# Performance work log

Measured on AMD Instinct MI355X. Metric: run time of the kernel, lower is better.

## Reference

```python
import jax, jax.numpy as jnp
import numpy as np

N_NODES = 100000

def setup_inputs() -> dict:
    key = jax.random.key(0)
    k = jax.random.split(key, 6)
    N, E, D = N_NODES, 1600000, 128
    x = jax.random.normal(k[0], (N, D), dtype=jnp.float32)
    edge_src = jax.random.randint(k[1], (E,), 0, N, dtype=jnp.int32)
    edge_dst = jax.random.randint(k[2], (E,), 0, N, dtype=jnp.int32)
    edge_weight = jax.random.uniform(k[3], (E,), dtype=jnp.float32)
    W1 = jax.random.normal(k[4], (D, D), dtype=jnp.float32) * (1.0 / np.sqrt(D))
    W2 = jax.random.normal(k[5], (D, D), dtype=jnp.float32) * (1.0 / np.sqrt(D))
    return {"x": x, "edge_src": edge_src, "edge_dst": edge_dst,
            "edge_weight": edge_weight, "W1": W1, "W2": W2}

def _graph_conv(x, W, src, dst, ew, n_nodes):
    # GraphConv: h = A @ (x @ W); A given as weighted edge list.
    h = x @ W                               # [N, D_out]
    msg = h[src] * ew[:, None]              # [E, D_out] gather + scale
    return jax.ops.segment_sum(msg, dst, num_segments=n_nodes)  # [N, D_out]

def reference(x, edge_src, edge_dst, edge_weight, W1, W2):
    n = x.shape[0]
    # layer 1: tanh(GraphConv) ; Dropout(0) is identity
    x = jnp.tanh(_graph_conv(x, W1, edge_src, edge_dst, edge_weight, n))
    # layer 2
    x = jnp.tanh(_graph_conv(x, W2, edge_src, edge_dst, edge_weight, n))
    return x
```

## Files before the change

### kernel.cpp

```cpp
#include <hip/hip_runtime.h>
#include <hip/hip_bf16.h>

#define N_NODES 100000
#define N_EDGES 1600000
#define D 128
#define BSZ 128
#define NBUCK 782
#define EPW 4096
#define NWG1 ((N_EDGES + EPW - 1) / EPW)
#define CAP 4096
#define OTS 272

typedef unsigned int  uint4n  __attribute__((ext_vector_type(4)));
typedef float         float4n __attribute__((ext_vector_type(4)));
typedef _Float16      half8n  __attribute__((ext_vector_type(8)));
typedef _Float16      half4n  __attribute__((ext_vector_type(4)));

#define SWZ(row, kb) (((row) << 8) + ((kb) ^ (((row) & 15) << 4)))

__device__ __forceinline__ float fast_tanh(float x) {
    float t = __builtin_amdgcn_exp2f(x * 2.885390081777927f);
    return 1.0f - 2.0f * __builtin_amdgcn_rcpf(t + 1.0f);
}

__global__ __launch_bounds__(256) void k_wprep_hist(const float* __restrict__ W1,
                                                    const float* __restrict__ W2,
                                                    char* __restrict__ Wt,
                                                    const int* __restrict__ dst,
                                                    int* __restrict__ bcnt) {
    if (blockIdx.x < 32) {
        const float* W = (blockIdx.x < 16) ? W1 : W2;
        char* dstp = Wt + ((blockIdx.x < 16) ? 0 : 32768);
        int t = (blockIdx.x & 15) * 256 + threadIdx.x;
        int idx = t * 4;
        int k = idx >> 7, c = idx & 127;
        float4 wv = *(const float4*)&W[idx];
        *(_Float16*)(dstp + SWZ(c + 0, k * 2)) = (_Float16)wv.x;
        *(_Float16*)(dstp + SWZ(c + 1, k * 2)) = (_Float16)wv.y;
        *(_Float16*)(dstp + SWZ(c + 2, k * 2)) = (_Float16)wv.z;
        *(_Float16*)(dstp + SWZ(c + 3, k * 2)) = (_Float16)wv.w;
        return;
    }
    __shared__ int h[NBUCK];
    for (int i = threadIdx.x; i < NBUCK; i += 256) h[i] = 0;
    __syncthreads();
    int hb   = blockIdx.x - 32;
    int base = hb * EPW;
    int end  = min(base + EPW, N_EDGES);
    int i = base + threadIdx.x;
    for (; i + 768 < end; i += 1024) {
        int d0 = dst[i], d1 = dst[i + 256], d2 = dst[i + 512], d3 = dst[i + 768];
        atomicAdd(&h[d0 >> 7], 1);
        atomicAdd(&h[d1 >> 7], 1);
        atomicAdd(&h[d2 >> 7], 1);
        atomicAdd(&h[d3 >> 7], 1);
    }
    for (; i < end; i += 256)
        atomicAdd(&h[dst[i] >> 7], 1);
    __syncthreads();
    for (int j = threadIdx.x; j < NBUCK; j += 256)
        if (h[j]) atomicAdd(&bcnt[j], h[j]);
}

__global__ void k_scanN(const int* __restrict__ bcnt, int* __restrict__ boff,
                        int* __restrict__ gcur) {
    __shared__ int tmp[256];
    int tid = threadIdx.x;
    int carry = 0;
    for (int c = 0; c < (NBUCK + 255) / 256; c++) {
        int i = c * 256 + tid;
        int v = (i < NBUCK) ? bcnt[i] : 0;
        tmp[tid] = v;
        __syncthreads();
        int run = v;
        for (int off = 1; off < 256; off <<= 1) {
            int t = (tid >= off) ? tmp[tid - off] : 0;
            __syncthreads();
            run += t;
            tmp[tid] = run;
            __syncthreads();
        }
        int excl = carry + run - v;
        if (i < NBUCK) { boff[i] = excl; gcur[i] = excl; }
        int tot = tmp[255];
        __syncthreads();
        carry += tot;
    }
    if (tid == 0) boff[NBUCK] = N_EDGES;
}

__global__ __launch_bounds__(256) void k_scat_gemm(const int* __restrict__ src,
                                                   const int* __restrict__ dst,
                                                   const float* __restrict__ ew,
                                                   int* __restrict__ gcur,
                                                   int2* __restrict__ ebuf,
                                                   const float* __restrict__ Xf,
                                                   const char* __restrict__ Wt,
                                                   _Float16* __restrict__ H, int n) {
    __shared__ char smem[17408];
    int tid = threadIdx.x;

    if (blockIdx.x < NWG1) {
        int* h  = (int*)smem;
        int* rb = h + NBUCK;
        for (int i = tid; i < NBUCK; i += 256) h[i] = 0;
        __syncthreads();
        int base = blockIdx.x * EPW;
        int end  = min(base + EPW, N_EDGES);
        {
            int i = base + tid;
            for (; i + 768 < end; i += 1024) {
                int d0 = dst[i], d1 = dst[i + 256], d2 = dst[i + 512], d3 = dst[i + 768];
                atomicAdd(&h[d0 >> 7], 1);
                atomicAdd(&h[d1 >> 7], 1);
                atomicAdd(&h[d2 >> 7], 1);
                atomicAdd(&h[d3 >> 7], 1);
            }
            for (; i < end; i += 256)
                atomicAdd(&h[dst[i] >> 7], 1);
        }
        __syncthreads();
        for (int i = tid; i < NBUCK; i += 256) {
            int c = h[i];
            if (c) rb[i] = atomicAdd(&gcur[i], c);
        }
        __syncthreads();
        {
            int i = base + tid;
            for (; i + 768 < end; i += 1024) {
                int d0 = dst[i], d1 = dst[i + 256], d2 = dst[i + 512], d3 = dst[i + 768];
                int s0 = src[i], s1 = src[i + 256], s2 = src[i + 512], s3 = src[i + 768];
                float w0 = ew[i], w1 = ew[i + 256], w2 = ew[i + 512], w3 = ew[i + 768];
                int p0 = atomicAdd(&rb[d0 >> 7], 1);
                int p1 = atomicAdd(&rb[d1 >> 7], 1);
                int p2 = atomicAdd(&rb[d2 >> 7], 1);
                int p3 = atomicAdd(&rb[d3 >> 7], 1);
                ebuf[p0] = make_int2((s0 << 8) | (d0 & 127), __float_as_int(w0));
                ebuf[p1] = make_int2((s1 << 8) | (d1 & 127), __float_as_int(w1));
                ebuf[p2] = make_int2((s2 << 8) | (d2 & 127), __float_as_int(w2));
                ebuf[p3] = make_int2((s3 << 8) | (d3 & 127), __float_as_int(w3));
            }
            for (; i < end; i += 256) {
                int d = dst[i];
                int p = atomicAdd(&rb[d >> 7], 1);
                ebuf[p] = make_int2((src[i] << 8) | (d & 127), __float_as_int(ew[i]));
            }
        }
        return;
    }

    char* sA = smem;
    int lane = tid & 63, w = tid >> 6;
    int rows0 = (blockIdx.x - NWG1) * 64;

    int rb2 = (w >> 1) * 32;
    int cb = (w & 1) * 64;
    int lr = lane & 15;
    int kg = (lane >> 4) * 16;

    #pragma unroll
    for (int rep = 0; rep < 8; rep++) {
        int ef = rep * 1024 + tid * 4;
        int r = ef >> 7, c = ef & 127;
        int rg = rows0 + r;
        float4 xv = make_float4(0.f, 0.f, 0.f, 0.f);
        if (rg < n) xv = *(const float4*)(Xf + (size_t)rg * 128 + c);
        half4n hv;
        hv[0] = (_Float16)xv.x; hv[1] = (_Float16)xv.y;
        hv[2] = (_Float16)xv.z; hv[3] = (_Float16)xv.w;
        *(half4n*)(sA + SWZ(r, c * 2)) = hv;
    }
    __syncthreads();

    float4n acc[2][4] = {};
    #pragma unroll
    for (int ks = 0; ks < 4; ks++) {
        half8n bwk[4];
        #pragma unroll
        for (int ct = 0; ct < 4; ct++)
            bwk[ct] = *(const half8n*)(Wt + SWZ(cb + ct * 16 + lr, ks * 64 + kg));
        half8n af[2];
        #pragma unroll
        for (int rt = 0; rt < 2; rt++)
            af[rt] = *(const half8n*)(sA + SWZ(rb2 + rt * 16 + lr, ks * 64 + kg));
        #pragma unroll
        for (int rt = 0; rt < 2; rt++)
            #pragma unroll
            for (int ct = 0; ct < 4; ct++)
                acc[rt][ct] = __builtin_amdgcn_mfma_f32_16x16x32_f16(af[rt], bwk[ct], acc[rt][ct], 0, 0, 0);
    }

    __syncthreads();
    char* OT = smem;
    int rloc = rb2 + (lane >> 4) * 4;
    #pragma unroll
    for (int rt = 0; rt < 2; rt++) {
        #pragma unroll
        for (int ct = 0; ct < 4; ct++) {
            int col = cb + ct * 16 + lr;
            #pragma unroll
            for (int r = 0; r < 4; r++)
                *(_Float16*)(OT + (rloc + rt * 16 + r) * OTS + col * 2) = (_Float16)acc[rt][ct][r];
        }
    }
    __syncthreads();
    #pragma unroll
    for (int rep = 0; rep < 4; rep++) {
        int ef = rep * 2048 + tid * 8;
        int r = ef >> 7, c = ef & 127;
        int rg = rows0 + r;
        if (rg < n) {
            half8n v = *(const half8n*)(OT + r * OTS + c * 2);
            *(half8n*)&H[(size_t)rg * 128 + c] = v;
        }
    }
}

__global__ __launch_bounds__(512) void k_sortb(int2* __restrict__ ebuf,
                                               const int* __restrict__ boff,
                                               int* __restrict__ rowptr) {
    __shared__ int2 se[CAP];
    __shared__ int cnt[BSZ];
    __shared__ int cur[BSZ];
    int tid = threadIdx.x;
    int b   = blockIdx.x;
    int e0 = boff[b], e1 = boff[b + 1];
    int m  = e1 - e0;
    if (tid < BSZ) cnt[tid] = 0;
    __syncthreads();
    int2 ovf;
    bool hasOvf = false;
    for (int i = tid; i < m; i += 512) {
        int2 v = ebuf[e0 + i];
        if (i < CAP) se[i] = v;
        else { ovf = v; hasOvf = true; }
        atomicAdd(&cnt[v.x & (BSZ - 1)], 1);
    }
    __syncthreads();
    if (tid < 64) {
        int a  = cnt[tid * 2], bq = cnt[tid * 2 + 1];
        int s  = a + bq;
        int incl = s;
        #pragma unroll
        for (int off = 1; off < 64; off <<= 1) {
            int t = __shfl_up(incl, off, 64);
            if (tid >= off) incl += t;
        }
        int ex = incl - s;
        cur[tid * 2]     = ex;
        cur[tid * 2 + 1] = ex + a;
        int node = b * BSZ + tid * 2;
        if (node     <= N_NODES) rowptr[node]     = e0 + ex;
        if (node + 1 <= N_NODES) rowptr[node + 1] = e0 + ex + a;
    }
    __syncthreads();
    for (int i = tid; i < m && i < CAP; i += 512) {
        int2 v = se[i];
        int p = atomicAdd(&cur[v.x & (BSZ - 1)], 1);
        ebuf[e0 + p] = v;
    }
    if (hasOvf) {
        int p = atomicAdd(&cur[ovf.x & (BSZ - 1)], 1);
        ebuf[e0 + p] = ovf;
    }
}

__global__ __launch_bounds__(256) void k_gemm2(const _Float16* __restrict__ Xh,
                                               const char* __restrict__ Wt,
                                               _Float16* __restrict__ H, int n) {
    __shared__ char smem[17408];
    char* sA = smem;
    int tid  = threadIdx.x;
    int lane = tid & 63, w = tid >> 6;
    int rows0 = blockIdx.x * 64;

    int rb = (w >> 1) * 32;
    int cb = (w & 1) * 64;
    int lr = lane & 15;
    int kg = (lane >> 4) * 16;

    #pragma unroll
    for (int rep = 0; rep < 4; rep++) {
        int ef = rep * 2048 + tid * 8;
        int r = ef >> 7, c = ef & 127;
        int rg = rows0 + r;
        half8n v = half8n(0);
        if (rg < n) v = *(const half8n*)(Xh + (size_t)rg * 128 + c);
        *(half8n*)(sA + SWZ(r, c * 2)) = v;
    }
    __syncthreads();

    float4n acc[2][4] = {};
    #pragma unroll
    for (int ks = 0; ks < 4; ks++) {
        half8n bwk[4];
        #pragma unroll
        for (int ct = 0; ct < 4; ct++)
            bwk[ct] = *(const half8n*)(Wt + SWZ(cb + ct * 16 + lr, ks * 64 + kg));
        half8n af[2];
        #pragma unroll
        for (int rt = 0; rt < 2; rt++)
            af[rt] = *(const half8n*)(sA + SWZ(rb + rt * 16 + lr, ks * 64 + kg));
        #pragma unroll
        for (int rt = 0; rt < 2; rt++)
            #pragma unroll
            for (int ct = 0; ct < 4; ct++)
                acc[rt][ct] = __builtin_amdgcn_mfma_f32_16x16x32_f16(af[rt], bwk[ct], acc[rt][ct], 0, 0, 0);
    }

    __syncthreads();
    char* OT = smem;
    int rloc = rb + (lane >> 4) * 4;
    #pragma unroll
    for (int rt = 0; rt < 2; rt++) {
        #pragma unroll
        for (int ct = 0; ct < 4; ct++) {
            int col = cb + ct * 16 + lr;
            #pragma unroll
            for (int r = 0; r < 4; r++)
                *(_Float16*)(OT + (rloc + rt * 16 + r) * OTS + col * 2) = (_Float16)acc[rt][ct][r];
        }
    }
    __syncthreads();
    #pragma unroll
    for (int rep = 0; rep < 4; rep++) {
        int ef = rep * 2048 + tid * 8;
        int r = ef >> 7, c = ef & 127;
        int rg = rows0 + r;
        if (rg < n) {
            half8n v = *(const half8n*)(OT + r * OTS + c * 2);
            *(half8n*)&H[(size_t)rg * 128 + c] = v;
        }
    }
}

template<bool OUTF16>
__global__ __launch_bounds__(256) void k_agg(const _Float16* __restrict__ H,
                                             const int* __restrict__ rowptr,
                                             const int2* __restrict__ ebuf,
                                             void* __restrict__ outv, int n) {
    int wv   = (blockIdx.x * 256 + threadIdx.x) >> 6;
    int lane = threadIdx.x & 63;
    int g = lane >> 4;
    int c = lane & 15;
    int node = wv * 4 + g;
    if (node >= n) return;
    const char* Hc = (const char*)H + (c << 4);
    int e0 = rowptr[node], e1 = rowptr[node + 1];
    float acc[8] = {};
    int e = e0;
    for (; e + 4 <= e1; e += 4) {
        int2 d0 = ebuf[e];
        int2 d1 = ebuf[e + 1];
        int2 d2 = ebuf[e + 2];
        int2 d3 = ebuf[e + 3];
        half8n v0 = *(const half8n*)(Hc + (size_t)((unsigned)d0.x & 0xFFFFFF00u));
        half8n v1 = *(const half8n*)(Hc + (size_t)((unsigned)d1.x & 0xFFFFFF00u));
        half8n v2 = *(const half8n*)(Hc + (size_t)((unsigned)d2.x & 0xFFFFFF00u));
        half8n v3 = *(const half8n*)(Hc + (size_t)((unsigned)d3.x & 0xFFFFFF00u));
        float w0 = __int_as_float(d0.y);
        float w1 = __int_as_float(d1.y);
        float w2 = __int_as_float(d2.y);
        float w3 = __int_as_float(d3.y);
        #pragma unroll
        for (int j = 0; j < 8; j++) acc[j] = __builtin_fmaf((float)v0[j], w0, acc[j]);
        #pragma unroll
        for (int j = 0; j < 8; j++) acc[j] = __builtin_fmaf((float)v1[j], w1, acc[j]);
        #pragma unroll
        for (int j = 0; j < 8; j++) acc[j] = __builtin_fmaf((float)v2[j], w2, acc[j]);
        #pragma unroll
        for (int j = 0; j < 8; j++) acc[j] = __builtin_fmaf((float)v3[j], w3, acc[j]);
    }
    for (; e < e1; ++e) {
        int2 ed = ebuf[e];
        half8n v = *(const half8n*)(Hc + (size_t)((unsigned)ed.x & 0xFFFFFF00u));
        float w = __int_as_float(ed.y);
        #pragma unroll
        for (int j = 0; j < 8; j++) acc[j] = __builtin_fmaf((float)v[j], w, acc[j]);
    }
    if (OUTF16) {
        half8n hv;
        #pragma unroll
        for (int j = 0; j < 8; j++) hv[j] = (_Float16)fast_tanh(acc[j]);
        *(uint4n*)((_Float16*)outv + (size_t)node * 128 + c * 8) = *(uint4n*)&hv;
    } else {
        float* op = (float*)outv + (size_t)node * 128 + c * 8;
        float4n o0, o1;
        o0.x = fast_tanh(acc[0]); o0.y = fast_tanh(acc[1]);
        o0.z = fast_tanh(acc[2]); o0.w = fast_tanh(acc[3]);
        o1.x = fast_tanh(acc[4]); o1.y = fast_tanh(acc[5]);
        o1.z = fast_tanh(acc[6]); o1.w = fast_tanh(acc[7]);
        __builtin_nontemporal_store(o0, (float4n*)op);
        __builtin_nontemporal_store(o1, (float4n*)(op + 4));
    }
}


extern "C" void kernel_launch(void* const* d_in, const int* in_sizes, int n_in,
                              void* d_out, int out_size, void* d_ws, size_t ws_size,
                              hipStream_t stream) {
    const float* x    = (const float*)d_in[0];
    const int*   esrc = (const int*)d_in[1];
    const int*   edst = (const int*)d_in[2];
    const float* ew   = (const float*)d_in[3];
    const float* W1   = (const float*)d_in[4];
    const float* W2   = (const float*)d_in[5];
    float* out = (float*)d_out;

    _Float16* hbuf = (_Float16*)d_ws;
    _Float16* act1 = hbuf + (size_t)N_NODES * D;
    int2* ebuf     = (int2*)(act1 + (size_t)N_NODES * D);
    int*  bcnt     = (int*)(ebuf + N_EDGES);
    int*  boff     = bcnt + NBUCK;
    int*  gcur     = boff + (NBUCK + 1);
    int*  rowptr   = gcur + NBUCK;
    char* Wt       = (char*)(rowptr + N_NODES + 8);
    (void)ws_size; (void)in_sizes; (void)n_in; (void)out_size;

    int gemm_blocks = (N_NODES + 63) / 64;
    int agg_blocks  = (N_NODES + 15) / 16;

    hipMemsetAsync(bcnt, 0, NBUCK * sizeof(int), stream);
    k_wprep_hist<<<32 + NWG1, 256, 0, stream>>>(W1, W2, Wt, edst, bcnt);
    k_scanN<<<1, 256, 0, stream>>>(bcnt, boff, gcur);
    k_scat_gemm<<<NWG1 + gemm_blocks, 256, 0, stream>>>(esrc, edst, ew, gcur, ebuf,
                                                        x, Wt, hbuf, N_NODES);
    k_sortb<<<NBUCK, 512, 0, stream>>>(ebuf, boff, rowptr);

    k_agg<true><<<agg_blocks, 256, 0, stream>>>(hbuf, rowptr, ebuf, act1, N_NODES);
    k_gemm2<<<gemm_blocks, 256, 0, stream>>>(act1, Wt + 32768, hbuf, N_NODES);
    k_agg<false><<<agg_blocks, 256, 0, stream>>>(hbuf, rowptr, ebuf, out, N_NODES);
}
```

Measured before the change: 219.3 us.

## Replace global histogram+atomic scatter with per-block local bucketing and staged merge

Removes the separate global histogram pass, memset and global atomic cursor. Instead each scatter block locally scans its bucket histogram and writes records to a private staging region, recording per-block counts and offsets. New column-sum and scan kernels compute the bucket offsets, and the sort kernel gathers each bucket's records from all blocks using a binary search over per-block prefix counts. This drops one full pass over dst and the global atomics, at the cost of more kernels, a 256-step in-block scan per scatter block, and a binary search per record in the sort.

```diff
diff --git a/kernel.cpp b/kernel.cpp
--- a/kernel.cpp
+++ b/kernel.cpp
@@ -23,77 +23,27 @@
     return 1.0f - 2.0f * __builtin_amdgcn_rcpf(t + 1.0f);
 }
 
-__global__ __launch_bounds__(256) void k_wprep_hist(const float* __restrict__ W1,
-                                                    const float* __restrict__ W2,
-                                                    char* __restrict__ Wt,
-                                                    const int* __restrict__ dst,
-                                                    int* __restrict__ bcnt) {
-    if (blockIdx.x < 32) {
-        const float* W = (blockIdx.x < 16) ? W1 : W2;
-        char* dstp = Wt + ((blockIdx.x < 16) ? 0 : 32768);
-        int t = (blockIdx.x & 15) * 256 + threadIdx.x;
-        int idx = t * 4;
-        int k = idx >> 7, c = idx & 127;
-        float4 wv = *(const float4*)&W[idx];
-        *(_Float16*)(dstp + SWZ(c + 0, k * 2)) = (_Float16)wv.x;
-        *(_Float16*)(dstp + SWZ(c + 1, k * 2)) = (_Float16)wv.y;
-        *(_Float16*)(dstp + SWZ(c + 2, k * 2)) = (_Float16)wv.z;
-        *(_Float16*)(dstp + SWZ(c + 3, k * 2)) = (_Float16)wv.w;
-        return;
-    }
-    __shared__ int h[NBUCK];
-    for (int i = threadIdx.x; i < NBUCK; i += 256) h[i] = 0;
-    __syncthreads();
-    int hb   = blockIdx.x - 32;
-    int base = hb * EPW;
-    int end  = min(base + EPW, N_EDGES);
-    int i = base + threadIdx.x;
-    for (; i + 768 < end; i += 1024) {
-        int d0 = dst[i], d1 = dst[i + 256], d2 = dst[i + 512], d3 = dst[i + 768];
-        atomicAdd(&h[d0 >> 7], 1);
-        atomicAdd(&h[d1 >> 7], 1);
-        atomicAdd(&h[d2 >> 7], 1);
-        atomicAdd(&h[d3 >> 7], 1);
-    }
-    for (; i < end; i += 256)
-        atomicAdd(&h[dst[i] >> 7], 1);
-    __syncthreads();
-    for (int j = threadIdx.x; j < NBUCK; j += 256)
-        if (h[j]) atomicAdd(&bcnt[j], h[j]);
-}
-
-__global__ void k_scanN(const int* __restrict__ bcnt, int* __restrict__ boff,
-                        int* __restrict__ gcur) {
-    __shared__ int tmp[256];
-    int tid = threadIdx.x;
-    int carry = 0;
-    for (int c = 0; c < (NBUCK + 255) / 256; c++) {
-        int i = c * 256 + tid;
-        int v = (i < NBUCK) ? bcnt[i] : 0;
-        tmp[tid] = v;
-        __syncthreads();
-        int run = v;
-        for (int off = 1; off < 256; off <<= 1) {
-            int t = (tid >= off) ? tmp[tid - off] : 0;
-            __syncthreads();
-            run += t;
-            tmp[tid] = run;
-            __syncthreads();
-        }
-        int excl = carry + run - v;
-        if (i < NBUCK) { boff[i] = excl; gcur[i] = excl; }
-        int tot = tmp[255];
-        __syncthreads();
-        carry += tot;
-    }
-    if (tid == 0) boff[NBUCK] = N_EDGES;
+__global__ __launch_bounds__(256) void k_wprep(const float* __restrict__ W1,
+                                               const float* __restrict__ W2,
+                                               char* __restrict__ Wt) {
+    const float* W = (blockIdx.x < 16) ? W1 : W2;
+    char* dstp = Wt + ((blockIdx.x < 16) ? 0 : 32768);
+    int t = (blockIdx.x & 15) * 256 + threadIdx.x;
+    int idx = t * 4;
+    int k = idx >> 7, c = idx & 127;
+    float4 wv = *(const float4*)&W[idx];
+    *(_Float16*)(dstp + SWZ(c + 0, k * 2)) = (_Float16)wv.x;
+    *(_Float16*)(dstp + SWZ(c + 1, k * 2)) = (_Float16)wv.y;
+    *(_Float16*)(dstp + SWZ(c + 2, k * 2)) = (_Float16)wv.z;
+    *(_Float16*)(dstp + SWZ(c + 3, k * 2)) = (_Float16)wv.w;
 }
 
 __global__ __launch_bounds__(256) void k_scat_gemm(const int* __restrict__ src,
                                                    const int* __restrict__ dst,
                                                    const float* __restrict__ ew,
-                                                   int* __restrict__ gcur,
-                                                   int2* __restrict__ ebuf,
+                                                   int2* __restrict__ staging,
+                                                   int* __restrict__ cntM,
+                                                   int* __restrict__ loffM,
                                                    const float* __restrict__ Xf,
                                                    const char* __restrict__ Wt,
                                                    _Float16* __restrict__ H, int n) {
@@ -101,11 +51,13 @@
     int tid = threadIdx.x;
 
     if (blockIdx.x < NWG1) {
-        int* h  = (int*)smem;
-        int* rb = h + NBUCK;
+        int* h   = (int*)smem;
+        int* cur = h + NBUCK;
+        int* tmp = cur + NBUCK;
+        int blk  = blockIdx.x;
         for (int i = tid; i < NBUCK; i += 256) h[i] = 0;
         __syncthreads();
-        int base = blockIdx.x * EPW;
+        int base = blk * EPW;
         int end  = min(base + EPW, N_EDGES);
         {
             int i = base + tid;
@@ -120,30 +72,51 @@
                 atomicAdd(&h[dst[i] >> 7], 1);
         }
         __syncthreads();
-        for (int i = tid; i < NBUCK; i += 256) {
-            int c = h[i];
-            if (c) rb[i] = atomicAdd(&gcur[i], c);
+        int carry = 0;
+        for (int c = 0; c < 4; c++) {
+            int i = c * 256 + tid;
+            int v = (i < NBUCK) ? h[i] : 0;
+            tmp[tid] = v;
+            __syncthreads();
+            int run = v;
+            for (int off = 1; off < 256; off <<= 1) {
+                int t = (tid >= off) ? tmp[tid - off] : 0;
+                __syncthreads();
+                run += t;
+                tmp[tid] = run;
+                __syncthreads();
+            }
+            int excl = carry + run - v;
+            if (i < NBUCK) {
+                cur[i] = excl;
+                cntM[blk * NBUCK + i]  = v;
+                loffM[blk * NBUCK + i] = excl;
+            }
+            int tot = tmp[255];
+            __syncthreads();
+            carry += tot;
         }
         __syncthreads();
         {
+            int2* sg = staging + (size_t)blk * EPW;
             int i = base + tid;
             for (; i + 768 < end; i += 1024) {
                 int d0 = dst[i], d1 = dst[i + 256], d2 = dst[i + 512], d3 = dst[i + 768];
                 int s0 = src[i], s1 = src[i + 256], s2 = src[i + 512], s3 = src[i + 768];
                 float w0 = ew[i], w1 = ew[i + 256], w2 = ew[i + 512], w3 = ew[i + 768];
-                int p0 = atomicAdd(&rb[d0 >> 7], 1);
-                int p1 = atomicAdd(&rb[d1 >> 7], 1);
-                int p2 = atomicAdd(&rb[d2 >> 7], 1);
-                int p3 = atomicAdd(&rb[d3 >> 7], 1);
-                ebuf[p0] = make_int2((s0 << 8) | (d0 & 127), __float_as_int(w0));
-                ebuf[p1] = make_int2((s1 << 8) | (d1 & 127), __float_as_int(w1));
-                ebuf[p2] = make_int2((s2 << 8) | (d2 & 127), __float_as_int(w2));
-                ebuf[p3] = make_int2((s3 << 8) | (d3 & 127), __float_as_int(w3));
+                int p0 = atomicAdd(&cur[d0 >> 7], 1);
+                int p1 = atomicAdd(&cur[d1 >> 7], 1);
+                int p2 = atomicAdd(&cur[d2 >> 7], 1);
+                int p3 = atomicAdd(&cur[d3 >> 7], 1);
+                sg[p0] = make_int2((s0 << 8) | (d0 & 127), __float_as_int(w0));
+                sg[p1] = make_int2((s1 << 8) | (d1 & 127), __float_as_int(w1));
+                sg[p2] = make_int2((s2 << 8) | (d2 & 127), __float_as_int(w2));
+                sg[p3] = make_int2((s3 << 8) | (d3 & 127), __float_as_int(w3));
             }
             for (; i < end; i += 256) {
                 int d = dst[i];
-                int p = atomicAdd(&rb[d >> 7], 1);
-                ebuf[p] = make_int2((src[i] << 8) | (d & 127), __float_as_int(ew[i]));
+                int p = atomicAdd(&cur[d >> 7], 1);
+                sg[p] = make_int2((src[i] << 8) | (d & 127), __float_as_int(ew[i]));
             }
         }
         return;
@@ -216,29 +189,91 @@
     }
 }
 
-__global__ __launch_bounds__(512) void k_sortb(int2* __restrict__ ebuf,
+__global__ __launch_bounds__(256) void k_sumcol(const int* __restrict__ cntM,
+                                                int* __restrict__ bcnt) {
+    int b = blockIdx.x * 256 + threadIdx.x;
+    if (b >= NBUCK) return;
+    int s = 0;
+    int blk = 0;
+    for (; blk + 4 <= NWG1; blk += 4) {
+        int a0 = cntM[(size_t)(blk + 0) * NBUCK + b];
+        int a1 = cntM[(size_t)(blk + 1) * NBUCK + b];
+        int a2 = cntM[(size_t)(blk + 2) * NBUCK + b];
+        int a3 = cntM[(size_t)(blk + 3) * NBUCK + b];
+        s += a0 + a1 + a2 + a3;
+    }
+    for (; blk < NWG1; blk++) s += cntM[(size_t)blk * NBUCK + b];
+    bcnt[b] = s;
+}
+
+__global__ void k_scanN(const int* __restrict__ bcnt, int* __restrict__ boff) {
+    __shared__ int tmp[256];
+    int tid = threadIdx.x;
+    int carry = 0;
+    for (int c = 0; c < (NBUCK + 255) / 256; c++) {
+        int i = c * 256 + tid;
+        int v = (i < NBUCK) ? bcnt[i] : 0;
+        tmp[tid] = v;
+        __syncthreads();
+        int run = v;
+        for (int off = 1; off < 256; off <<= 1) {
+            int t = (tid >= off) ? tmp[tid - off] : 0;
+            __syncthreads();
+            run += t;
+            tmp[tid] = run;
+            __syncthreads();
+        }
+        int excl = carry + run - v;
+        if (i < NBUCK) boff[i] = excl;
+        int tot = tmp[255];
+        __syncthreads();
+        carry += tot;
+    }
+    if (tid == 0) boff[NBUCK] = N_EDGES;
+}
+
+__global__ __launch_bounds__(512) void k_sortb(const int2* __restrict__ staging,
+                                               const int* __restrict__ cntM,
+                                               const int* __restrict__ loffM,
                                                const int* __restrict__ boff,
+                                               int2* __restrict__ ebuf,
                                                int* __restrict__ rowptr) {
     __shared__ int2 se[CAP];
-    __shared__ int cnt[BSZ];
-    __shared__ int cur[BSZ];
+    __shared__ int rcs[512];
+    __shared__ int rco[512];
+    __shared__ int lfs[NWG1];
+    __shared__ int cnt2[BSZ];
+    __shared__ int cur2[BSZ];
     int tid = threadIdx.x;
     int b   = blockIdx.x;
     int e0 = boff[b], e1 = boff[b + 1];
     int m  = e1 - e0;
-    if (tid < BSZ) cnt[tid] = 0;
-    __syncthreads();
-    int2 ovf;
-    bool hasOvf = false;
+    {
+        int v = (tid < NWG1) ? cntM[(size_t)tid * NBUCK + b] : 0;
+        rcs[tid] = v;
+        rco[tid] = v;
+        if (tid < NWG1) lfs[tid] = loffM[(size_t)tid * NBUCK + b];
+        if (tid < BSZ) cnt2[tid] = 0;
+    }
+    __syncthreads();
+    for (int off = 1; off < 512; off <<= 1) {
+        int t = (tid >= off) ? rcs[tid - off] : 0;
+        __syncthreads();
+        rcs[tid] += t;
+        __syncthreads();
+    }
     for (int i = tid; i < m; i += 512) {
-        int2 v = ebuf[e0 + i];
-        if (i < CAP) se[i] = v;
-        else { ovf = v; hasOvf = true; }
-        atomicAdd(&cnt[v.x & (BSZ - 1)], 1);
+        int lo = 0, hi = NWG1 - 1;
+        while (lo < hi) { int mid = (lo + hi) >> 1; if (rcs[mid] > i) hi = mid; else lo = mid + 1; }
+        int blk = lo;
+        int within = i - (rcs[blk] - rco[blk]);
+        int2 rec = staging[(size_t)blk * EPW + lfs[blk] + within];
+        if (i < CAP) se[i] = rec;
+        atomicAdd(&cnt2[rec.x & (BSZ - 1)], 1);
     }
     __syncthreads();
     if (tid < 64) {
-        int a  = cnt[tid * 2], bq = cnt[tid * 2 + 1];
+        int a  = cnt2[tid * 2], bq = cnt2[tid * 2 + 1];
         int s  = a + bq;
         int incl = s;
         #pragma unroll
@@ -247,21 +282,24 @@
             if (tid >= off) incl += t;
         }
         int ex = incl - s;
-        cur[tid * 2]     = ex;
-        cur[tid * 2 + 1] = ex + a;
+        cur2[tid * 2]     = ex;
+        cur2[tid * 2 + 1] = ex + a;
         int node = b * BSZ + tid * 2;
         if (node     <= N_NODES) rowptr[node]     = e0 + ex;
         if (node + 1 <= N_NODES) rowptr[node + 1] = e0 + ex + a;
     }
     __syncthreads();
-    for (int i = tid; i < m && i < CAP; i += 512) {
-        int2 v = se[i];
-        int p = atomicAdd(&cur[v.x & (BSZ - 1)], 1);
-        ebuf[e0 + p] = v;
-    }
-    if (hasOvf) {
-        int p = atomicAdd(&cur[ovf.x & (BSZ - 1)], 1);
-        ebuf[e0 + p] = ovf;
+    for (int i = tid; i < m; i += 512) {
+        int2 rec;
+        if (i < CAP) rec = se[i];
+        else {
+            int lo = 0, hi = NWG1 - 1;
+            while (lo < hi) { int mid = (lo + hi) >> 1; if (rcs[mid] > i) hi = mid; else lo = mid + 1; }
+            int blk = lo;
+            rec = staging[(size_t)blk * EPW + lfs[blk] + (i - (rcs[blk] - rco[blk]))];
+        }
+        int p = atomicAdd(&cur2[rec.x & (BSZ - 1)], 1);
+        ebuf[e0 + p] = rec;
     }
 }
 
@@ -409,23 +447,26 @@
 
     _Float16* hbuf = (_Float16*)d_ws;
     _Float16* act1 = hbuf + (size_t)N_NODES * D;
+    int2* staging  = (int2*)act1;
+    int*  cntM     = (int*)(staging + (size_t)NWG1 * EPW);
+    int*  loffM    = cntM + (size_t)NWG1 * NBUCK;
     int2* ebuf     = (int2*)(act1 + (size_t)N_NODES * D);
     int*  bcnt     = (int*)(ebuf + N_EDGES);
     int*  boff     = bcnt + NBUCK;
-    int*  gcur     = boff + (NBUCK + 1);
-    int*  rowptr   = gcur + NBUCK;
+    int*  rowptr   = boff + (NBUCK + 2);
     char* Wt       = (char*)(rowptr + N_NODES + 8);
     (void)ws_size; (void)in_sizes; (void)n_in; (void)out_size;
 
     int gemm_blocks = (N_NODES + 63) / 64;
     int agg_blocks  = (N_NODES + 15) / 16;
 
-    hipMemsetAsync(bcnt, 0, NBUCK * sizeof(int), stream);
-    k_wprep_hist<<<32 + NWG1, 256, 0, stream>>>(W1, W2, Wt, edst, bcnt);
-    k_scanN<<<1, 256, 0, stream>>>(bcnt, boff, gcur);
-    k_scat_gemm<<<NWG1 + gemm_blocks, 256, 0, stream>>>(esrc, edst, ew, gcur, ebuf,
+    k_wprep<<<32, 256, 0, stream>>>(W1, W2, Wt);
+    k_scat_gemm<<<NWG1 + gemm_blocks, 256, 0, stream>>>(esrc, edst, ew,
+                                                        staging, cntM, loffM,
                                                         x, Wt, hbuf, N_NODES);
-    k_sortb<<<NBUCK, 512, 0, stream>>>(ebuf, boff, rowptr);
+    k_sumcol<<<(NBUCK + 255) / 256, 256, 0, stream>>>(cntM, bcnt);
+    k_scanN<<<1, 256, 0, stream>>>(bcnt, boff);
+    k_sortb<<<NBUCK, 512, 0, stream>>>(staging, cntM, loffM, boff, ebuf, rowptr);
 
     k_agg<true><<<agg_blocks, 256, 0, stream>>>(hbuf, rowptr, ebuf, act1, N_NODES);
     k_gemm2<<<gemm_blocks, 256, 0, stream>>>(act1, Wt + 32768, hbuf, N_NODES);
```

Result: faster. 210.6 us (median of 2 runs) (-3.9%).
